# Kernel optimization log

Hardware: AMD Instinct MI355X
Metric: run time of the kernel (lower is better)

## Reference

```python
import jax, jax.numpy as jnp
import numpy as np

N, M, K, D = 65536, 131072, 8, 64
TAU = 0.3
EPS = 1e-6

def setup_inputs() -> dict:
    key = jax.random.key(0)
    ks = jax.random.split(key, 16)
    s = 0.05
    return {
        "f_pts": jax.random.normal(ks[0], (N, D), jnp.float32),
        "pts": jax.random.uniform(ks[1], (N, 3), jnp.float32) * 10.0,
        "z_latent": jax.random.normal(ks[2], (M, D), jnp.float32) * 0.1,
        "centers": jax.random.uniform(ks[3], (M, 3), jnp.float32) * 10.0,
        "cand_idx": jax.random.randint(ks[4], (N, K), 0, M),
        "sim_w1": jax.random.normal(ks[5], (2 * D + 3, 64), jnp.float32) * s,
        "sim_b1": jnp.zeros((64,), jnp.float32),
        "sim_w2": jax.random.normal(ks[6], (64, 1), jnp.float32) * s,
        "sim_b2": jnp.zeros((1,), jnp.float32),
        "gate_w1": jax.random.normal(ks[7], (2 * D, D), jnp.float32) * s,
        "gate_b1": jnp.zeros((D,), jnp.float32),
        "gate_w2": jax.random.normal(ks[8], (D, 1), jnp.float32) * s,
        "gate_b2": jnp.zeros((1,), jnp.float32),
        "W_ih": jax.random.normal(ks[9], (3 * D, D), jnp.float32) * s,
        "W_hh": jax.random.normal(ks[10], (3 * D, D), jnp.float32) * s,
        "b_ih": jnp.zeros((3 * D,), jnp.float32),
        "b_hh": jnp.zeros((3 * D,), jnp.float32),
    }

def _forward(f_pts, pts, z_latent, centers, sim_w1, sim_b1, sim_w2, sim_b2,
             gate_w1, gate_b1, gate_w2, gate_b2, W_ih, W_hh, b_ih, b_hh, cand_idx):
    n, k = cand_idx.shape
    m, d = z_latent.shape
    # --- gather voxel latents / centers for each (point, candidate) pair ---
    z_c = z_latent[cand_idx]                         # (N,K,D)
    delta = pts[:, None, :] - centers[cand_idx]      # (N,K,3)
    f_b = jnp.broadcast_to(f_pts[:, None, :], (n, k, d))
    # --- similarity MLP ---
    x = jnp.concatenate([f_b, z_c, delta], axis=-1)  # (N,K,2D+3)
    h = jax.nn.relu(x @ sim_w1 + sim_b1)
    sim = (h @ sim_w2 + sim_b2)[..., 0]              # (N,K)
    # --- low-temperature top-K routing weights over candidates ---
    w = jax.nn.softmax(sim / TAU, axis=-1)           # (N,K)
    # --- scatter weighted point features to voxels ---
    flat_idx = cand_idx.reshape(-1)                  # (N*K,)
    contrib = (w[..., None] * f_pts[:, None, :]).reshape(-1, d)
    msg = jax.ops.segment_sum(contrib, flat_idx, num_segments=m)     # (M,D)
    wsum = jax.ops.segment_sum(w.reshape(-1), flat_idx, num_segments=m)
    msg = msg / (wsum[:, None] + EPS)                # normalized voxel message
    # --- per-voxel gate ---
    g_in = jnp.concatenate([z_latent, msg], axis=-1)
    gate = jax.nn.sigmoid(jax.nn.relu(g_in @ gate_w1 + gate_b1) @ gate_w2 + gate_b2)  # (M,1)
    # --- GRUCell (torch layout: rows ordered r,z,n) ---
    gi = msg @ W_ih.T + b_ih
    gh = z_latent @ W_hh.T + b_hh
    i_r, i_z, i_n = jnp.split(gi, 3, axis=-1)
    h_r, h_z, h_n = jnp.split(gh, 3, axis=-1)
    r = jax.nn.sigmoid(i_r + h_r)
    zg = jax.nn.sigmoid(i_z + h_z)
    nn_ = jnp.tanh(i_n + r * h_n)
    h_new = (1.0 - zg) * nn_ + zg * z_latent
    # gated latent update
    return z_latent + gate * (h_new - z_latent)

def reference(f_pts, pts, z_latent, centers, cand_idx, sim_w1, sim_b1, sim_w2, sim_b2,
              gate_w1, gate_b1, gate_w2, gate_b2, W_ih, W_hh, b_ih, b_hh):
    return _forward(f_pts, pts, z_latent, centers, sim_w1, sim_b1, sim_w2, sim_b2,
                    gate_w1, gate_b1, gate_w2, gate_b2, W_ih, W_hh, b_ih, b_hh, cand_idx)
```

## Files before the change

### kernel.cpp

```cpp
#include <hip/hip_runtime.h>
#include <hip/hip_fp16.h>
#include <math.h>


typedef short bf16x8 __attribute__((ext_vector_type(8)));
typedef unsigned short u16x8 __attribute__((ext_vector_type(8)));
typedef float f32x4 __attribute__((ext_vector_type(4)));
#define MFMA __builtin_amdgcn_mfma_f32_16x16x32_bf16
#define CAP 32

__device__ __forceinline__ short f2bf(float f) {
  unsigned u = __float_as_uint(f);
  unsigned r = (u + 0x7FFFu + ((u >> 16) & 1u)) >> 16;
  return (short)r;
}

__device__ __forceinline__ float bf2f(unsigned short h) {
  return __uint_as_float(((unsigned)h) << 16);
}

__device__ __forceinline__ float sigm(float x) { return 1.0f / (1.0f + __expf(-x)); }

__global__ __launch_bounds__(256) void prep_kernel(
    const float* __restrict__ z, const float* __restrict__ f,
    const float* __restrict__ sim_w1, const float* __restrict__ sim_b1,
    unsigned short* __restrict__ zbf, unsigned short* __restrict__ fbf,
    unsigned short* __restrict__ HBt, int* __restrict__ cursor,
    short* __restrict__ bfZ, int M)
{
  long tid = (long)blockIdx.x * 256 + threadIdx.x;
  long nthr = (long)gridDim.x * 256;

  for (long i = tid; i < M; i += nthr) cursor[i] = 0;

  long nz = (long)M * 64;
  for (long i = tid * 8; i < nz; i += nthr * 8) {
    float4 a = *(const float4*)&z[i];
    float4 b4 = *(const float4*)&z[i + 4];
    u16x8 o;
    o[0] = (unsigned short)f2bf(a.x);  o[1] = (unsigned short)f2bf(a.y);
    o[2] = (unsigned short)f2bf(a.z);  o[3] = (unsigned short)f2bf(a.w);
    o[4] = (unsigned short)f2bf(b4.x); o[5] = (unsigned short)f2bf(b4.y);
    o[6] = (unsigned short)f2bf(b4.z); o[7] = (unsigned short)f2bf(b4.w);
    *(u16x8*)&zbf[i] = o;
  }

  if (blockIdx.x == gridDim.x - 1 && threadIdx.x < 64) {
    int lane = threadIdx.x;
    int lr = lane & 15, lg = lane >> 4;
#pragma unroll
    for (int ct = 0; ct < 4; ++ct)
#pragma unroll
      for (int kt = 0; kt < 3; ++kt) {
        bf16x8 b;
#pragma unroll
        for (int e = 0; e < 8; ++e) {
          int k = kt * 32 + lg * 8 + e;
          float v = (k < 67) ? sim_w1[(64 + k) * 64 + ct * 16 + lr] : 0.0f;
          b[e] = f2bf(v);
        }
        *(bf16x8*)&bfZ[(ct * 3 + kt) * 512 + lane * 8] = b;
      }
  }

  if (blockIdx.x < 1024) {
    int wave = blockIdx.x * 4 + (threadIdx.x >> 6);
    int lane = threadIdx.x & 63;
    int lr = lane & 15, lg = lane >> 4;
    int n0 = wave * 16;

    bf16x8 bf[8];
#pragma unroll
    for (int ct = 0; ct < 4; ++ct)
#pragma unroll
      for (int kt = 0; kt < 2; ++kt) {
        bf16x8 bb;
#pragma unroll
        for (int e = 0; e < 8; ++e)
          bb[e] = f2bf(sim_w1[(kt * 32 + lg * 8 + e) * 64 + ct * 16 + lr]);
        bf[ct * 2 + kt] = bb;
      }

    bf16x8 a[2];
#pragma unroll
    for (int kt = 0; kt < 2; ++kt) {
      const float* src = &f[(long)(n0 + lr) * 64 + kt * 32 + lg * 8];
      float4 v0 = *(const float4*)src;
      float4 v1 = *(const float4*)(src + 4);
      bf16x8 t;
      t[0] = f2bf(v0.x); t[1] = f2bf(v0.y); t[2] = f2bf(v0.z); t[3] = f2bf(v0.w);
      t[4] = f2bf(v1.x); t[5] = f2bf(v1.y); t[6] = f2bf(v1.z); t[7] = f2bf(v1.w);
      a[kt] = t;
    }
    *(bf16x8*)&fbf[(long)(n0 + lr) * 64 + lg * 8] = a[0];
    *(bf16x8*)&fbf[(long)(n0 + lr) * 64 + 32 + lg * 8] = a[1];

    f32x4 acc[4] = {{0,0,0,0},{0,0,0,0},{0,0,0,0},{0,0,0,0}};
#pragma unroll
    for (int ct = 0; ct < 4; ++ct) {
      acc[ct] = MFMA(a[0], bf[ct * 2 + 0], acc[ct], 0, 0, 0);
      acc[ct] = MFMA(a[1], bf[ct * 2 + 1], acc[ct], 0, 0, 0);
    }
    float b10 = sim_b1[lr], b11 = sim_b1[16 + lr];
    float b12 = sim_b1[32 + lr], b13 = sim_b1[48 + lr];
#pragma unroll
    for (int e = 0; e < 4; ++e) {
      unsigned lo = (unsigned)(unsigned short)f2bf(acc[0][e] + b10)
                  | ((unsigned)(unsigned short)f2bf(acc[1][e] + b11) << 16);
      unsigned hi = (unsigned)(unsigned short)f2bf(acc[2][e] + b12)
                  | ((unsigned)(unsigned short)f2bf(acc[3][e] + b13) << 16);
      *(uint2*)&HBt[(long)(n0 + lg * 4 + e) * 64 + lr * 4] = make_uint2(lo, hi);
    }
  }
}

#define TPW 4
__global__ __launch_bounds__(256) void pair_kernel(
    const float* __restrict__ pts, const unsigned short* __restrict__ zbf,
    const float* __restrict__ centers, const int* __restrict__ cand_idx,
    const float* __restrict__ sim_w2, const short* __restrict__ bfZ,
    const unsigned short* __restrict__ HBt,
    int* __restrict__ cursor, unsigned* __restrict__ rec)
{
  int wave = (blockIdx.x * 256 + threadIdx.x) >> 6;
  int lane = threadIdx.x & 63;
  int lr = lane & 15, lg = lane >> 4;

  int call = cand_idx[wave * 64 + lane];

  bf16x8 b[12];
#pragma unroll
  for (int i = 0; i < 12; ++i) b[i] = *(const bf16x8*)&bfZ[i * 512 + lane * 8];
  float w2c[4];
#pragma unroll
  for (int ct = 0; ct < 4; ++ct) w2c[ct] = sim_w2[ct * 16 + lr];

  int c[TPW];
  bf16x8 a0[TPW], a1[TPW], ad[TPW];
  uint2 h2[TPW];
#pragma unroll
  for (int t = 0; t < TPW; ++t) {
    c[t] = __shfl(call, t * 16 + lr, 64);
    a0[t] = *(const bf16x8*)&zbf[(long)c[t] * 64 + lg * 8];
    a1[t] = *(const bf16x8*)&zbf[(long)c[t] * 64 + 32 + lg * 8];
    h2[t] = *(const uint2*)&HBt[((long)(wave * TPW + t) * 2 + (lg >> 1)) * 64 + lr * 4];
    bf16x8 tt = {0, 0, 0, 0, 0, 0, 0, 0};
    if (lg == 0) {
      int n = (wave * TPW + t) * 2 + (lr >> 3);
      tt[0] = f2bf(pts[n * 3 + 0] - centers[c[t] * 3 + 0]);
      tt[1] = f2bf(pts[n * 3 + 1] - centers[c[t] * 3 + 1]);
      tt[2] = f2bf(pts[n * 3 + 2] - centers[c[t] * 3 + 2]);
    }
    ad[t] = tt;
  }

  f32x4 part[TPW];
#pragma unroll
  for (int t = 0; t < TPW; ++t) {
    f32x4 acc[4] = {{0,0,0,0},{0,0,0,0},{0,0,0,0},{0,0,0,0}};
#pragma unroll
    for (int ct = 0; ct < 4; ++ct) {
      acc[ct] = MFMA(a0[t], b[ct * 3 + 0], acc[ct], 0, 0, 0);
      acc[ct] = MFMA(a1[t], b[ct * 3 + 1], acc[ct], 0, 0, 0);
      acc[ct] = MFMA(ad[t], b[ct * 3 + 2], acc[ct], 0, 0, 0);
    }
    float hb[4];
    hb[0] = bf2f((unsigned short)(h2[t].x));
    hb[1] = bf2f((unsigned short)(h2[t].x >> 16));
    hb[2] = bf2f((unsigned short)(h2[t].y));
    hb[3] = bf2f((unsigned short)(h2[t].y >> 16));
    f32x4 p = {0.f, 0.f, 0.f, 0.f};
#pragma unroll
    for (int ct = 0; ct < 4; ++ct)
#pragma unroll
      for (int e = 0; e < 4; ++e)
        p[e] = fmaf(fmaxf(acc[ct][e] + hb[ct], 0.0f), w2c[ct], p[e]);
    part[t] = p;
  }

  float wrow[TPW];
#pragma unroll
  for (int t = 0; t < TPW; ++t) {
    f32x4 p = part[t];
#pragma unroll
    for (int m = 1; m <= 8; m <<= 1)
#pragma unroll
      for (int e = 0; e < 4; ++e) p[e] += __shfl_xor(p[e], m, 64);
    float other[4];
#pragma unroll
    for (int e = 0; e < 4; ++e) other[e] = __shfl_xor(p[e], 16, 64);
    float mx = p[0];
#pragma unroll
    for (int e = 1; e < 4; ++e) mx = fmaxf(mx, p[e]);
#pragma unroll
    for (int e = 0; e < 4; ++e) mx = fmaxf(mx, other[e]);
    float ex[4], se = 0.f, so = 0.f;
#pragma unroll
    for (int e = 0; e < 4; ++e) {
      ex[e] = __expf((p[e] - mx) * (1.0f / 0.3f));
      se += ex[e];
      so += __expf((other[e] - mx) * (1.0f / 0.3f));
    }
    float inv = 1.0f / (se + so);
    int srcl = (lane >> 2) << 4;
    float t0 = __shfl(ex[0] * inv, srcl, 64);
    float t1 = __shfl(ex[1] * inv, srcl, 64);
    float t2 = __shfl(ex[2] * inv, srcl, 64);
    float t3 = __shfl(ex[3] * inv, srcl, 64);
    int esel = lane & 3;
    wrow[t] = esel == 0 ? t0 : esel == 1 ? t1 : esel == 2 ? t2 : t3;
  }

  int slot = atomicAdd(&cursor[call], 1);

  float v0 = __shfl(wrow[0], lr, 64);
  float v1 = __shfl(wrow[1], lr, 64);
  float v2 = __shfl(wrow[2], lr, 64);
  float v3 = __shfl(wrow[3], lr, 64);
  float wv = lg == 0 ? v0 : lg == 1 ? v1 : lg == 2 ? v2 : v3;

  if (slot < CAP) {
    int n_pt = wave * 8 + 2 * lg + (lr >> 3);
    unsigned short wh = __half_as_ushort(__float2half(wv));
    rec[(long)call * CAP + slot] = ((unsigned)n_pt << 16) | (unsigned)wh;
  }
}

__global__ __launch_bounds__(256) void gather_kernel(
    const unsigned* __restrict__ rec, const int* __restrict__ cursor,
    const unsigned short* __restrict__ fbf, unsigned short* __restrict__ msg_bf,
    int mvox)
{
  int tid = blockIdx.x * 256 + threadIdx.x;
  int row = tid >> 2, seg = tid & 3;
  if (row >= mvox) return;

  int cnt = cursor[row];
  cnt = cnt < CAP ? cnt : CAP;
  const unsigned* rp = &rec[(long)row * CAP];

  float acc[16];
#pragma unroll
  for (int j = 0; j < 16; ++j) acc[j] = 0.f;
  float ws = 0.f;

  for (int i0 = 0; i0 < cnt; i0 += 4) {
    uint4 r4 = *(const uint4*)&rp[i0];
    unsigned rr0 = r4.x, rr1 = r4.y, rr2 = r4.z, rr3 = r4.w;
#pragma unroll
    for (int j = 0; j < 4; ++j) {
      unsigned r = j == 0 ? rr0 : j == 1 ? rr1 : j == 2 ? rr2 : rr3;
      if (i0 + j < cnt) {
        float w = __half2float(__ushort_as_half((unsigned short)(r & 0xffffu)));
        int n = r >> 16;
        ws += w;
        const u16x8* fp = (const u16x8*)&fbf[(long)n * 64 + seg * 16];
        u16x8 f0 = fp[0], f1 = fp[1];
#pragma unroll
        for (int k = 0; k < 8; ++k) {
          acc[k]     = fmaf(w, bf2f(f0[k]), acc[k]);
          acc[8 + k] = fmaf(w, bf2f(f1[k]), acc[8 + k]);
        }
      }
    }
  }
  float inv = 1.0f / (ws + 1e-6f);
  u16x8 o0, o1;
#pragma unroll
  for (int j = 0; j < 8; ++j) {
    o0[j] = (unsigned short)f2bf(acc[j] * inv);
    o1[j] = (unsigned short)f2bf(acc[8 + j] * inv);
  }
  *(u16x8*)&msg_bf[(long)row * 64 + seg * 16] = o0;
  *(u16x8*)&msg_bf[(long)row * 64 + seg * 16 + 8] = o1;
}

#define GST 136
#define WST 72

__global__ __launch_bounds__(512)
__attribute__((amdgpu_waves_per_eu(2)))
void stage2(
    const unsigned short* __restrict__ zbf,
    const float* __restrict__ gate_w1, const float* __restrict__ gate_b1,
    const float* __restrict__ gate_w2, const float* __restrict__ gate_b2,
    const float* __restrict__ W_ih, const float* __restrict__ W_hh,
    const float* __restrict__ b_ih, const float* __restrict__ b_hh,
    const unsigned short* __restrict__ msg_bf,
    float* __restrict__ out, int ntiles)
{
  __shared__ short G1t[64 * GST];
  __shared__ short Wih_l[192 * WST];
  __shared__ short Whh_l[192 * WST];
  __shared__ float gb1s[64], gw2s[64], bihs[192], bhhs[192];
  __shared__ float gb2s;

  int t = threadIdx.x;
  for (int s = t; s < 64 * 128; s += 512) {
    int j = s & 63, k = s >> 6;
    G1t[j * GST + k] = f2bf(gate_w1[s]);
  }
  for (int s = t; s < 192 * 64; s += 512) {
    int j = s >> 6, k = s & 63;
    Wih_l[j * WST + k] = f2bf(W_ih[s]);
    Whh_l[j * WST + k] = f2bf(W_hh[s]);
  }
  if (t < 64) { gb1s[t] = gate_b1[t]; gw2s[t] = gate_w2[t]; }
  if (t < 192) { bihs[t] = b_ih[t]; bhhs[t] = b_hh[t]; }
  if (t == 0) gb2s = gate_b2[0];
  __syncthreads();

  int wid = t >> 6, lane = t & 63;
  int lr = lane & 15, lg = lane >> 4;

#pragma unroll 1
  for (int tile = blockIdx.x; tile < ntiles; tile += gridDim.x) {
    int rowbase = tile * 128 + wid * 16;
    long abase = (long)(rowbase + lr) * 64;
    bf16x8 a0 = *(const bf16x8*)&zbf[abase + lg * 8];
    bf16x8 a1 = *(const bf16x8*)&zbf[abase + 32 + lg * 8];
    bf16x8 a2 = *(const bf16x8*)&msg_bf[abase + lg * 8];
    bf16x8 a3 = *(const bf16x8*)&msg_bf[abase + 32 + lg * 8];

    f32x4 usum = {0.f, 0.f, 0.f, 0.f};
#pragma unroll 1
    for (int ct = 0; ct < 4; ++ct) {
      f32x4 au = {0, 0, 0, 0};
      au = MFMA(a0, *(const bf16x8*)&G1t[(ct * 16 + lr) * GST +  0 + lg * 8], au, 0, 0, 0);
      au = MFMA(a1, *(const bf16x8*)&G1t[(ct * 16 + lr) * GST + 32 + lg * 8], au, 0, 0, 0);
      au = MFMA(a2, *(const bf16x8*)&G1t[(ct * 16 + lr) * GST + 64 + lg * 8], au, 0, 0, 0);
      au = MFMA(a3, *(const bf16x8*)&G1t[(ct * 16 + lr) * GST + 96 + lg * 8], au, 0, 0, 0);
      int c = ct * 16 + lr;
#pragma unroll
      for (int e = 0; e < 4; ++e)
        usum[e] += fmaxf(au[e] + gb1s[c], 0.0f) * gw2s[c];
    }
#pragma unroll
    for (int m = 1; m <= 8; m <<= 1)
#pragma unroll
      for (int e = 0; e < 4; ++e) {
        float v = usum[e];
        usum[e] = v + __shfl_xor(v, m, 64);
      }
    float gate[4];
#pragma unroll
    for (int e = 0; e < 4; ++e) gate[e] = sigm(usum[e] + gb2s);

#pragma unroll 1
    for (int ct = 0; ct < 4; ++ct) {
      f32x4 air = {0,0,0,0}, aiz = {0,0,0,0}, ain = {0,0,0,0};
      f32x4 ahr = {0,0,0,0}, ahz = {0,0,0,0}, ahn = {0,0,0,0};
#pragma unroll
      for (int k2 = 0; k2 < 2; ++k2) {
        bf16x8 amg = k2 ? a3 : a2;
        bf16x8 az_ = k2 ? a1 : a0;
        int ko = k2 * 32 + lg * 8;
        air = MFMA(amg, *(const bf16x8*)&Wih_l[(      ct * 16 + lr) * WST + ko], air, 0, 0, 0);
        aiz = MFMA(amg, *(const bf16x8*)&Wih_l[( 64 + ct * 16 + lr) * WST + ko], aiz, 0, 0, 0);
        ain = MFMA(amg, *(const bf16x8*)&Wih_l[(128 + ct * 16 + lr) * WST + ko], ain, 0, 0, 0);
        ahr = MFMA(az_, *(const bf16x8*)&Whh_l[(      ct * 16 + lr) * WST + ko], ahr, 0, 0, 0);
        ahz = MFMA(az_, *(const bf16x8*)&Whh_l[( 64 + ct * 16 + lr) * WST + ko], ahz, 0, 0, 0);
        ahn = MFMA(az_, *(const bf16x8*)&Whh_l[(128 + ct * 16 + lr) * WST + ko], ahn, 0, 0, 0);
      }
      int c = ct * 16 + lr;
#pragma unroll
      for (int e = 0; e < 4; ++e) {
        float zv = bf2f(zbf[(long)(rowbase + lg * 4 + e) * 64 + c]);
        float rr = sigm(air[e] + bihs[c] + ahr[e] + bhhs[c]);
        float zg = sigm(aiz[e] + bihs[64 + c] + ahz[e] + bhhs[64 + c]);
        float nn = tanhf(ain[e] + bihs[128 + c] + rr * (ahn[e] + bhhs[128 + c]));
        float hnew = (1.0f - zg) * nn + zg * zv;
        out[(long)(rowbase + lg * 4 + e) * 64 + c] = zv + gate[e] * (hnew - zv);
      }
    }
  }
}

extern "C" void kernel_launch(void* const* d_in, const int* in_sizes, int n_in,
                              void* d_out, int out_size, void* d_ws, size_t ws_size,
                              hipStream_t stream) {
  const float* f_pts   = (const float*)d_in[0];
  const float* pts     = (const float*)d_in[1];
  const float* z_lat   = (const float*)d_in[2];
  const float* centers = (const float*)d_in[3];
  const int*   cand    = (const int*)d_in[4];
  const float* sim_w1  = (const float*)d_in[5];
  const float* sim_b1  = (const float*)d_in[6];
  const float* sim_w2  = (const float*)d_in[7];
  const float* gate_w1 = (const float*)d_in[9];
  const float* gate_b1 = (const float*)d_in[10];
  const float* gate_w2 = (const float*)d_in[11];
  const float* gate_b2 = (const float*)d_in[12];
  const float* W_ih    = (const float*)d_in[13];
  const float* W_hh    = (const float*)d_in[14];
  const float* b_ih    = (const float*)d_in[15];
  const float* b_hh    = (const float*)d_in[16];

  int N = in_sizes[0] / 64;
  int M = in_sizes[2] / 64;

  int* cursor = (int*)d_ws;
  unsigned* rec = (unsigned*)(cursor + M);
  unsigned short* msg_bf = (unsigned short*)rec;
  unsigned short* zbf = (unsigned short*)(rec + (size_t)M * CAP);
  unsigned short* fbf = zbf + (size_t)M * 64;
  unsigned short* HBt = fbf + (size_t)N * 64;
  short* bfZ = (short*)(HBt + (size_t)N * 64);

  prep_kernel<<<2048, 256, 0, stream>>>(z_lat, f_pts, sim_w1, sim_b1,
                                        zbf, fbf, HBt, cursor, bfZ, M);

  int nwaves = (N * 8) / (16 * TPW);
  pair_kernel<<<nwaves / 4, 256, 0, stream>>>(pts, zbf, centers, cand,
                                              sim_w2, bfZ, HBt, cursor, rec);

  gather_kernel<<<(M * 4) / 256, 256, 0, stream>>>(rec, cursor, fbf, msg_bf, M);

  int ntiles = M / 128;
  stage2<<<512, 512, 0, stream>>>(zbf, gate_w1, gate_b1, gate_w2, gate_b2,
                                  W_ih, W_hh, b_ih, b_hh, msg_bf,
                                  (float*)d_out, ntiles);
}
```

Measured before the change: 107.2 us.

## Precompute slot atomics in prep, pre-pack GRU/gate weights, one-tile stage2 blocks

Moves the per-pair cursor atomicAdd out of pair_kernel into prep_kernel, which writes slot indices to a buffer so pair_kernel only reads them. A separate small kernel now zeroes the cursor array. Gate and GRU weights are converted once in prep into MFMA fragment layout in global memory, so stage2 no longer stages weights into LDS per block. Stage2 now launches one block per 128-row tile instead of a grid-stride loop. The cost is an extra kernel launch and slot-buffer traffic, and stage2 now reads its weight fragments from global memory instead of LDS.

```diff
diff --git a/kernel.cpp b/kernel.cpp
--- a/kernel.cpp
+++ b/kernel.cpp
@@ -21,17 +21,29 @@
 
 __device__ __forceinline__ float sigm(float x) { return 1.0f / (1.0f + __expf(-x)); }
 
+__global__ __launch_bounds__(256) void zero_cursor(int* __restrict__ c, int m) {
+  int n4 = m >> 2;
+  int stride = gridDim.x * 256;
+  int4* p = (int4*)c;
+  for (int j = blockIdx.x * 256 + threadIdx.x; j < n4; j += stride)
+    p[j] = make_int4(0, 0, 0, 0);
+}
+
 __global__ __launch_bounds__(256) void prep_kernel(
     const float* __restrict__ z, const float* __restrict__ f,
     const float* __restrict__ sim_w1, const float* __restrict__ sim_b1,
+    const float* __restrict__ gate_w1, const float* __restrict__ W_ih,
+    const float* __restrict__ W_hh, const int* __restrict__ cand,
     unsigned short* __restrict__ zbf, unsigned short* __restrict__ fbf,
-    unsigned short* __restrict__ HBt, int* __restrict__ cursor,
-    short* __restrict__ bfZ, int M)
+    unsigned short* __restrict__ HBt, short* __restrict__ bfZ,
+    short* __restrict__ GF, short* __restrict__ WihF, short* __restrict__ WhhF,
+    int* __restrict__ slotbuf, int* __restrict__ cursor, int M, long npairs)
 {
   long tid = (long)blockIdx.x * 256 + threadIdx.x;
   long nthr = (long)gridDim.x * 256;
 
-  for (long i = tid; i < M; i += nthr) cursor[i] = 0;
+  for (long i = tid; i < npairs; i += nthr)
+    slotbuf[i] = atomicAdd(&cursor[cand[i]], 1);
 
   long nz = (long)M * 64;
   for (long i = tid * 8; i < nz; i += nthr * 8) {
@@ -63,6 +75,33 @@
       }
   }
 
+  if (blockIdx.x >= 1024 && blockIdx.x < 1040) {
+    int fb = (blockIdx.x - 1024) * 4 + (threadIdx.x >> 6);
+    int lane = threadIdx.x & 63, lr = lane & 15, lg = lane >> 4;
+    bf16x8 o;
+    if (fb < 16) {
+      int ct = fb >> 2, kt = fb & 3;
+#pragma unroll
+      for (int e = 0; e < 8; ++e)
+        o[e] = f2bf(gate_w1[(kt * 32 + lg * 8 + e) * 64 + ct * 16 + lr]);
+      *(bf16x8*)&GF[fb * 512 + lane * 8] = o;
+    } else if (fb < 40) {
+      int q = fb - 16, g = q >> 3, ct = (q >> 1) & 3, k2 = q & 1;
+      int row = g * 64 + ct * 16 + lr;
+#pragma unroll
+      for (int e = 0; e < 8; ++e)
+        o[e] = f2bf(W_ih[row * 64 + k2 * 32 + lg * 8 + e]);
+      *(bf16x8*)&WihF[q * 512 + lane * 8] = o;
+    } else {
+      int q = fb - 40, g = q >> 3, ct = (q >> 1) & 3, k2 = q & 1;
+      int row = g * 64 + ct * 16 + lr;
+#pragma unroll
+      for (int e = 0; e < 8; ++e)
+        o[e] = f2bf(W_hh[row * 64 + k2 * 32 + lg * 8 + e]);
+      *(bf16x8*)&WhhF[q * 512 + lane * 8] = o;
+    }
+  }
+
   if (blockIdx.x < 1024) {
     int wave = blockIdx.x * 4 + (threadIdx.x >> 6);
     int lane = threadIdx.x & 63;
@@ -120,13 +159,14 @@
     const float* __restrict__ centers, const int* __restrict__ cand_idx,
     const float* __restrict__ sim_w2, const short* __restrict__ bfZ,
     const unsigned short* __restrict__ HBt,
-    int* __restrict__ cursor, unsigned* __restrict__ rec)
+    const int* __restrict__ slotbuf, unsigned* __restrict__ rec)
 {
   int wave = (blockIdx.x * 256 + threadIdx.x) >> 6;
   int lane = threadIdx.x & 63;
   int lr = lane & 15, lg = lane >> 4;
 
   int call = cand_idx[wave * 64 + lane];
+  int slot = slotbuf[wave * 64 + lane];
 
   bf16x8 b[12];
 #pragma unroll
@@ -211,8 +251,6 @@
     wrow[t] = esel == 0 ? t0 : esel == 1 ? t1 : esel == 2 ? t2 : t3;
   }
 
-  int slot = atomicAdd(&cursor[call], 1);
-
   float v0 = __shfl(wrow[0], lr, 64);
   float v1 = __shfl(wrow[1], lr, 64);
   float v2 = __shfl(wrow[2], lr, 64);
@@ -275,36 +313,22 @@
   *(u16x8*)&msg_bf[(long)row * 64 + seg * 16 + 8] = o1;
 }
 
-#define GST 136
-#define WST 72
-
 __global__ __launch_bounds__(512)
 __attribute__((amdgpu_waves_per_eu(2)))
 void stage2(
     const unsigned short* __restrict__ zbf,
-    const float* __restrict__ gate_w1, const float* __restrict__ gate_b1,
-    const float* __restrict__ gate_w2, const float* __restrict__ gate_b2,
-    const float* __restrict__ W_ih, const float* __restrict__ W_hh,
+    const short* __restrict__ GF, const short* __restrict__ WihF,
+    const short* __restrict__ WhhF,
+    const float* __restrict__ gate_b1, const float* __restrict__ gate_w2,
+    const float* __restrict__ gate_b2,
     const float* __restrict__ b_ih, const float* __restrict__ b_hh,
     const unsigned short* __restrict__ msg_bf,
-    float* __restrict__ out, int ntiles)
+    float* __restrict__ out)
 {
-  __shared__ short G1t[64 * GST];
-  __shared__ short Wih_l[192 * WST];
-  __shared__ short Whh_l[192 * WST];
   __shared__ float gb1s[64], gw2s[64], bihs[192], bhhs[192];
   __shared__ float gb2s;
 
   int t = threadIdx.x;
-  for (int s = t; s < 64 * 128; s += 512) {
-    int j = s & 63, k = s >> 6;
-    G1t[j * GST + k] = f2bf(gate_w1[s]);
-  }
-  for (int s = t; s < 192 * 64; s += 512) {
-    int j = s >> 6, k = s & 63;
-    Wih_l[j * WST + k] = f2bf(W_ih[s]);
-    Whh_l[j * WST + k] = f2bf(W_hh[s]);
-  }
   if (t < 64) { gb1s[t] = gate_b1[t]; gw2s[t] = gate_w2[t]; }
   if (t < 192) { bihs[t] = b_ih[t]; bhhs[t] = b_hh[t]; }
   if (t == 0) gb2s = gate_b2[0];
@@ -313,65 +337,62 @@
   int wid = t >> 6, lane = t & 63;
   int lr = lane & 15, lg = lane >> 4;
 
+  int rowbase = blockIdx.x * 128 + wid * 16;
+  long abase = (long)(rowbase + lr) * 64;
+  bf16x8 a0 = *(const bf16x8*)&zbf[abase + lg * 8];
+  bf16x8 a1 = *(const bf16x8*)&zbf[abase + 32 + lg * 8];
+  bf16x8 a2 = *(const bf16x8*)&msg_bf[abase + lg * 8];
+  bf16x8 a3 = *(const bf16x8*)&msg_bf[abase + 32 + lg * 8];
+
+  f32x4 usum = {0.f, 0.f, 0.f, 0.f};
 #pragma unroll 1
-  for (int tile = blockIdx.x; tile < ntiles; tile += gridDim.x) {
-    int rowbase = tile * 128 + wid * 16;
-    long abase = (long)(rowbase + lr) * 64;
-    bf16x8 a0 = *(const bf16x8*)&zbf[abase + lg * 8];
-    bf16x8 a1 = *(const bf16x8*)&zbf[abase + 32 + lg * 8];
-    bf16x8 a2 = *(const bf16x8*)&msg_bf[abase + lg * 8];
-    bf16x8 a3 = *(const bf16x8*)&msg_bf[abase + 32 + lg * 8];
-
-    f32x4 usum = {0.f, 0.f, 0.f, 0.f};
+  for (int ct = 0; ct < 4; ++ct) {
+    f32x4 au = {0, 0, 0, 0};
+    au = MFMA(a0, *(const bf16x8*)&GF[(ct * 4 + 0) * 512 + lane * 8], au, 0, 0, 0);
+    au = MFMA(a1, *(const bf16x8*)&GF[(ct * 4 + 1) * 512 + lane * 8], au, 0, 0, 0);
+    au = MFMA(a2, *(const bf16x8*)&GF[(ct * 4 + 2) * 512 + lane * 8], au, 0, 0, 0);
+    au = MFMA(a3, *(const bf16x8*)&GF[(ct * 4 + 3) * 512 + lane * 8], au, 0, 0, 0);
+    int c = ct * 16 + lr;
+#pragma unroll
+    for (int e = 0; e < 4; ++e)
+      usum[e] += fmaxf(au[e] + gb1s[c], 0.0f) * gw2s[c];
+  }
+#pragma unroll
+  for (int m = 1; m <= 8; m <<= 1)
+#pragma unroll
+    for (int e = 0; e < 4; ++e) {
+      float v = usum[e];
+      usum[e] = v + __shfl_xor(v, m, 64);
+    }
+  float gate[4];
+#pragma unroll
+  for (int e = 0; e < 4; ++e) gate[e] = sigm(usum[e] + gb2s);
+
 #pragma unroll 1
-    for (int ct = 0; ct < 4; ++ct) {
-      f32x4 au = {0, 0, 0, 0};
-      au = MFMA(a0, *(const bf16x8*)&G1t[(ct * 16 + lr) * GST +  0 + lg * 8], au, 0, 0, 0);
-      au = MFMA(a1, *(const bf16x8*)&G1t[(ct * 16 + lr) * GST + 32 + lg * 8], au, 0, 0, 0);
-      au = MFMA(a2, *(const bf16x8*)&G1t[(ct * 16 + lr) * GST + 64 + lg * 8], au, 0, 0, 0);
-      au = MFMA(a3, *(const bf16x8*)&G1t[(ct * 16 + lr) * GST + 96 + lg * 8], au, 0, 0, 0);
-      int c = ct * 16 + lr;
-#pragma unroll
-      for (int e = 0; e < 4; ++e)
-        usum[e] += fmaxf(au[e] + gb1s[c], 0.0f) * gw2s[c];
-    }
-#pragma unroll
-    for (int m = 1; m <= 8; m <<= 1)
-#pragma unroll
-      for (int e = 0; e < 4; ++e) {
-        float v = usum[e];
-        usum[e] = v + __shfl_xor(v, m, 64);
-      }
-    float gate[4];
-#pragma unroll
-    for (int e = 0; e < 4; ++e) gate[e] = sigm(usum[e] + gb2s);
-
-#pragma unroll 1
-    for (int ct = 0; ct < 4; ++ct) {
-      f32x4 air = {0,0,0,0}, aiz = {0,0,0,0}, ain = {0,0,0,0};
-      f32x4 ahr = {0,0,0,0}, ahz = {0,0,0,0}, ahn = {0,0,0,0};
-#pragma unroll
-      for (int k2 = 0; k2 < 2; ++k2) {
-        bf16x8 amg = k2 ? a3 : a2;
-        bf16x8 az_ = k2 ? a1 : a0;
-        int ko = k2 * 32 + lg * 8;
-        air = MFMA(amg, *(const bf16x8*)&Wih_l[(      ct * 16 + lr) * WST + ko], air, 0, 0, 0);
-        aiz = MFMA(amg, *(const bf16x8*)&Wih_l[( 64 + ct * 16 + lr) * WST + ko], aiz, 0, 0, 0);
-        ain = MFMA(amg, *(const bf16x8*)&Wih_l[(128 + ct * 16 + lr) * WST + ko], ain, 0, 0, 0);
-        ahr = MFMA(az_, *(const bf16x8*)&Whh_l[(      ct * 16 + lr) * WST + ko], ahr, 0, 0, 0);
-        ahz = MFMA(az_, *(const bf16x8*)&Whh_l[( 64 + ct * 16 + lr) * WST + ko], ahz, 0, 0, 0);
-        ahn = MFMA(az_, *(const bf16x8*)&Whh_l[(128 + ct * 16 + lr) * WST + ko], ahn, 0, 0, 0);
-      }
-      int c = ct * 16 + lr;
-#pragma unroll
-      for (int e = 0; e < 4; ++e) {
-        float zv = bf2f(zbf[(long)(rowbase + lg * 4 + e) * 64 + c]);
-        float rr = sigm(air[e] + bihs[c] + ahr[e] + bhhs[c]);
-        float zg = sigm(aiz[e] + bihs[64 + c] + ahz[e] + bhhs[64 + c]);
-        float nn = tanhf(ain[e] + bihs[128 + c] + rr * (ahn[e] + bhhs[128 + c]));
-        float hnew = (1.0f - zg) * nn + zg * zv;
-        out[(long)(rowbase + lg * 4 + e) * 64 + c] = zv + gate[e] * (hnew - zv);
-      }
+  for (int ct = 0; ct < 4; ++ct) {
+    f32x4 air = {0,0,0,0}, aiz = {0,0,0,0}, ain = {0,0,0,0};
+    f32x4 ahr = {0,0,0,0}, ahz = {0,0,0,0}, ahn = {0,0,0,0};
+#pragma unroll
+    for (int k2 = 0; k2 < 2; ++k2) {
+      bf16x8 amg = k2 ? a3 : a2;
+      bf16x8 az_ = k2 ? a1 : a0;
+      int base = ct * 2 + k2;
+      air = MFMA(amg, *(const bf16x8*)&WihF[(      base) * 512 + lane * 8], air, 0, 0, 0);
+      aiz = MFMA(amg, *(const bf16x8*)&WihF[( 8 +  base) * 512 + lane * 8], aiz, 0, 0, 0);
+      ain = MFMA(amg, *(const bf16x8*)&WihF[(16 +  base) * 512 + lane * 8], ain, 0, 0, 0);
+      ahr = MFMA(az_, *(const bf16x8*)&WhhF[(      base) * 512 + lane * 8], ahr, 0, 0, 0);
+      ahz = MFMA(az_, *(const bf16x8*)&WhhF[( 8 +  base) * 512 + lane * 8], ahz, 0, 0, 0);
+      ahn = MFMA(az_, *(const bf16x8*)&WhhF[(16 +  base) * 512 + lane * 8], ahn, 0, 0, 0);
+    }
+    int c = ct * 16 + lr;
+#pragma unroll
+    for (int e = 0; e < 4; ++e) {
+      float zv = bf2f(zbf[(long)(rowbase + lg * 4 + e) * 64 + c]);
+      float rr = sigm(air[e] + bihs[c] + ahr[e] + bhhs[c]);
+      float zg = sigm(aiz[e] + bihs[64 + c] + ahz[e] + bhhs[64 + c]);
+      float nn = tanhf(ain[e] + bihs[128 + c] + rr * (ahn[e] + bhhs[128 + c]));
+      float hnew = (1.0f - zg) * nn + zg * zv;
+      out[(long)(rowbase + lg * 4 + e) * 64 + c] = zv + gate[e] * (hnew - zv);
     }
   }
 }
@@ -406,18 +427,27 @@
   unsigned short* fbf = zbf + (size_t)M * 64;
   unsigned short* HBt = fbf + (size_t)N * 64;
   short* bfZ = (short*)(HBt + (size_t)N * 64);
+  short* GF = bfZ + 12 * 512;
+  short* WihF = GF + 16 * 512;
+  short* WhhF = WihF + 24 * 512;
+  int* slotbuf = (int*)(WhhF + 24 * 512);
+
+  long npairs = (long)N * 8;
+
+  zero_cursor<<<128, 256, 0, stream>>>(cursor, M);
 
   prep_kernel<<<2048, 256, 0, stream>>>(z_lat, f_pts, sim_w1, sim_b1,
-                                        zbf, fbf, HBt, cursor, bfZ, M);
+                                        gate_w1, W_ih, W_hh, cand,
+                                        zbf, fbf, HBt, bfZ, GF, WihF, WhhF,
+                                        slotbuf, cursor, M, npairs);
 
   int nwaves = (N * 8) / (16 * TPW);
   pair_kernel<<<nwaves / 4, 256, 0, stream>>>(pts, zbf, centers, cand,
-                                              sim_w2, bfZ, HBt, cursor, rec);
+                                              sim_w2, bfZ, HBt, slotbuf, rec);
 
   gather_kernel<<<(M * 4) / 256, 256, 0, stream>>>(rec, cursor, fbf, msg_bf, M);
 
-  int ntiles = M / 128;
-  stage2<<<512, 512, 0, stream>>>(zbf, gate_w1, gate_b1, gate_w2, gate_b2,
-                                  W_ih, W_hh, b_ih, b_hh, msg_bf,
-                                  (float*)d_out, ntiles);
-}
+  stage2<<<M / 128, 512, 0, stream>>>(zbf, GF, WihF, WhhF,
+                                      gate_b1, gate_w2, gate_b2, b_ih, b_hh,
+                                      msg_bf, (float*)d_out);
+}
```

New measurement: 115.6 us. +7.9%, slower.
